# Performance work log

Hardware: AMD Instinct MI355X
Metric: run time of the kernel (lower is better)

## Reference

```python
import jax, jax.numpy as jnp
import numpy as np

EPS_NORM = 1e-12


def _sage_layer(h, src, dst, n_dst, W_self, W_neigh, b):
    # DGL SAGEConv(mean) on a bipartite block: dst nodes = first n_dst src nodes.
    h_dst = h[:n_dst]
    msgs = h[src]                                              # [E, d] irregular gather
    s = jax.ops.segment_sum(msgs, dst, num_segments=n_dst)    # [n_dst, d]
    cnt = jax.ops.segment_sum(jnp.ones((src.shape[0],), h.dtype), dst, num_segments=n_dst)
    agg = s / jnp.maximum(cnt, 1.0)[:, None]                   # mean over in-neighbors (0-deg -> 0)
    out = h_dst @ W_self + agg @ W_neigh + b
    out = jax.nn.relu(out)                                     # activation=F.relu
    nrm = jnp.maximum(jnp.linalg.norm(out, axis=1, keepdims=True), EPS_NORM)
    return out / nrm                                           # norm=F.normalize


def setup_inputs() -> dict:
    key = jax.random.key(0)
    ks = jax.random.split(key, 16)
    N0, N1, N2 = 200000, 50000, 10000
    E0, E1 = 800000, 160000
    F_IN, H, L = 128, 256, 32
    x = jax.random.uniform(ks[0], (N0, F_IN), dtype=jnp.float32)
    src0 = jax.random.randint(ks[1], (E0,), 0, N0, dtype=jnp.int32)
    dst0 = jax.random.randint(ks[2], (E0,), 0, N1, dtype=jnp.int32)
    src1 = jax.random.randint(ks[3], (E1,), 0, N1, dtype=jnp.int32)
    dst1 = jax.random.randint(ks[4], (E1,), 0, N2, dtype=jnp.int32)
    sc = 0.05
    return {
        "x": x,
        "W_self0": jax.random.normal(ks[5], (F_IN, H), jnp.float32) * sc,
        "W_neigh0": jax.random.normal(ks[6], (F_IN, H), jnp.float32) * sc,
        "b0": jnp.zeros((H,), jnp.float32),
        "W_self1": jax.random.normal(ks[7], (H, H), jnp.float32) * sc,
        "W_neigh1": jax.random.normal(ks[8], (H, H), jnp.float32) * sc,
        "b1": jnp.zeros((H,), jnp.float32),
        "W_mu": jax.random.normal(ks[9], (H, L), jnp.float32) * sc,
        "b_mu": jnp.zeros((L,), jnp.float32),
        "W_var": jax.random.normal(ks[10], (H, L), jnp.float32) * sc,
        "b_var": jnp.zeros((L,), jnp.float32),
        "src0": src0, "dst0": dst0, "src1": src1, "dst1": dst1,
        "n_dst0": N1, "n_dst1": N2,
    }


def reference(x, W_self0, W_neigh0, b0, W_self1, W_neigh1, b1,
              W_mu, b_mu, W_var, b_var,
              src0, dst0, src1, dst1, n_dst0, n_dst1):
    h = jnp.log(x + 1.0)
    h = _sage_layer(h, src0, dst0, n_dst0, W_self0, W_neigh0, b0)
    h = _sage_layer(h, src1, dst1, n_dst1, W_self1, W_neigh1, b1)
    z_loc = h @ W_mu + b_mu
    z_scale = jnp.exp(h @ W_var + b_var) + 1e-6
    return (z_loc, z_scale)
```

## Files before the change

kernel.cpp:

```cpp
#include <hip/hip_runtime.h>
#include <math.h>

#define DEVI static __device__ __forceinline__

typedef __attribute__((ext_vector_type(8))) short s16x8;
typedef __attribute__((ext_vector_type(4))) float f32x4;

constexpr int CH = 4096;
constexpr int PADS = 3840;

DEVI float bf2f(unsigned short u) {
  union { unsigned int i; float f; } v; v.i = ((unsigned int)u) << 16; return v.f;
}
DEVI unsigned short f2bf(float f) {
  union { float f; unsigned int i; } v; v.f = f;
  return (unsigned short)((v.i + 0x7fffu + ((v.i >> 16) & 1u)) >> 16);
}

DEVI float fast_log1p(float x) {
  float t = x + 1.0f;
  float l;
  asm("v_log_f32 %0, %1" : "=v"(l) : "v"(t));
  return l * 0.6931471805599453f;
}

DEVI void log1p_span(const float* __restrict__ x, unsigned short* __restrict__ h0,
                     int lo, int hi, int blk, int nblk) {
  int bs = blockDim.x;
  int stride = nblk * bs;
  for (int i = lo + blk * bs + threadIdx.x; i < hi; i += stride) {
    float4 v = ((const float4*)x)[i];
    ushort4 o;
    o.x = f2bf(fast_log1p(v.x)); o.y = f2bf(fast_log1p(v.y));
    o.z = f2bf(fast_log1p(v.z)); o.w = f2bf(fast_log1p(v.w));
    ((ushort4*)h0)[i] = o;
  }
}

__global__ __launch_bounds__(256) void front_k(const int* __restrict__ dst0, int E0,
                                               const int* __restrict__ dst1, int E1,
                                               unsigned* __restrict__ gh, int B0, int B1,
                                               const float* __restrict__ Ws0, const float* __restrict__ Wn0,
                                               const float* __restrict__ Ws1, const float* __restrict__ Wn1,
                                               const float* __restrict__ Wmu, const float* __restrict__ Wvar,
                                               unsigned short* __restrict__ T0s, unsigned short* __restrict__ T0n,
                                               unsigned short* __restrict__ T1s, unsigned short* __restrict__ T1n,
                                               unsigned short* __restrict__ Thead,
                                               unsigned short* __restrict__ h1z, int N0, int N1,
                                               const float* __restrict__ x, unsigned short* __restrict__ h0,
                                               int lo, int hi, int LA) {
  __shared__ unsigned h[256];
  int b = blockIdx.x;
  int t = threadIdx.x;
  int BH = B0 + B1;
  if (b < BH) {
    bool L1 = b >= B0;
    const int* dst = L1 ? dst1 : dst0;
    int E = L1 ? E1 : E0;
    int base = L1 ? b - B0 : b;
    unsigned* out = L1 ? gh + 256 * B0 : gh;
    int B = L1 ? B1 : B0;
    h[t] = 0;
    __syncthreads();
    int e0 = base * CH, eend = min(e0 + CH, E);
    for (int i = e0 + t; i < eend; i += 256) atomicAdd(&h[((unsigned)dst[i]) >> 8], 1u);
    __syncthreads();
    out[t * B + base] = h[t];
  } else if (b < BH + 256) {
    if (b == BH) {
      if (t < 64) ((unsigned*)h0)[(size_t)N0 * 64 + t] = 0u;
      if (t < 128) ((unsigned*)h1z)[(size_t)N1 * 128 + t] = 0u;
    }
    int i = (b - BH) * 256 + t;
    if (i < 32768) {
      int hh = i >> 7, k = i & 127;
      T0s[i] = f2bf(Ws0[k * 256 + hh]);
      T0n[i] = f2bf(Wn0[k * 256 + hh]);
    }
    if (i < 65536) {
      int hh = i >> 8, k = i & 255;
      T1s[i] = f2bf(Ws1[k * 256 + hh]);
      T1n[i] = f2bf(Wn1[k * 256 + hh]);
    }
    if (i < 16384) {
      int c = i >> 8, k = i & 255;
      Thead[i] = f2bf(c < 32 ? Wmu[k * 32 + c] : Wvar[k * 32 + (c - 32)]);
    }
  } else {
    log1p_span(x, h0, lo, hi, b - BH - 256, LA);
  }
}

__global__ __launch_bounds__(256) void scan_sums_k(const unsigned* __restrict__ a, int NB,
                                                   unsigned* __restrict__ part,
                                                   const float* __restrict__ x, unsigned short* __restrict__ h0,
                                                   int lo, int hi, int LB) {
  __shared__ unsigned sm[256];
  int b = blockIdx.x, t = threadIdx.x;
  if (b >= NB) { log1p_span(x, h0, lo, hi, b - NB, LB); return; }
  sm[t] = a[b * 256 + t];
  __syncthreads();
  for (int o = 128; o > 0; o >>= 1) {
    if (t < o) sm[t] += sm[t + o];
    __syncthreads();
  }
  if (t == 0) part[b] = sm[0];
}

__global__ __launch_bounds__(256) void scan_write_k(unsigned* __restrict__ a, int NB,
                                                    const unsigned* __restrict__ part,
                                                    const float* __restrict__ x, unsigned short* __restrict__ h0,
                                                    int lo, int hi, int LC) {
  __shared__ unsigned sm[256];
  int b = blockIdx.x, t = threadIdx.x;
  if (b >= NB) { log1p_span(x, h0, lo, hi, b - NB, LC); return; }
  unsigned pv = (t < NB) ? part[t] : 0u;
  sm[t] = pv;
  __syncthreads();
  for (int o = 1; o < 256; o <<= 1) {
    unsigned xv = (t >= o) ? sm[t - o] : 0u;
    __syncthreads();
    sm[t] += xv;
    __syncthreads();
  }
  unsigned pb = (b == 0) ? 0u : sm[b - 1];
  __syncthreads();
  unsigned v = a[b * 256 + t];
  sm[t] = v;
  __syncthreads();
  for (int o = 1; o < 256; o <<= 1) {
    unsigned xv = (t >= o) ? sm[t - o] : 0u;
    __syncthreads();
    sm[t] += xv;
    __syncthreads();
  }
  a[b * 256 + t] = pb + sm[t] - v;
}

__global__ __launch_bounds__(1024) void scatter2_k(const int* __restrict__ src0, const int* __restrict__ dst0, int E0,
                                                   const int* __restrict__ src1, const int* __restrict__ dst1, int E1,
                                                   const unsigned* __restrict__ gh, int B0, int B1,
                                                   uint2* __restrict__ tmp,
                                                   const float* __restrict__ x, unsigned short* __restrict__ h0,
                                                   int lo, int hi, int LS) {
  __shared__ unsigned cur[256];
  int b = blockIdx.x;
  int NB = B0 + B1;
  if (b >= NB) { log1p_span(x, h0, lo, hi, b - NB, LS); return; }
  bool L1 = b >= B0;
  const int* dst = L1 ? dst1 : dst0;
  const int* src = L1 ? src1 : src0;
  int E = L1 ? E1 : E0;
  int base = L1 ? b - B0 : b;
  const unsigned* g = L1 ? gh + 256 * B0 : gh;
  int B = L1 ? B1 : B0;
  int t = threadIdx.x;
  if (t < 256) cur[t] = g[t * B + base];
  __syncthreads();
  int e0 = base * CH, eend = min(e0 + CH, E);
  for (int i = e0 + t; i < eend; i += 1024) {
    int d = dst[i];
    unsigned p = atomicAdd(&cur[((unsigned)d) >> 8], 1u);
    tmp[p] = make_uint2((unsigned)d, (unsigned)src[i]);
  }
}

__global__ __launch_bounds__(1024) void finalize_k(const uint2* __restrict__ tmp, const unsigned* __restrict__ gh,
                                                   int B0, int B1, int N1, int N2,
                                                   unsigned* __restrict__ off, unsigned* __restrict__ cnt,
                                                   int* __restrict__ ss, int QB0, int QB1,
                                                   int sent0, int sent1,
                                                   const float* __restrict__ x, unsigned short* __restrict__ h0,
                                                   int lo, int hi, int LF) {
  __shared__ unsigned h[256];
  __shared__ unsigned sm[256];
  __shared__ unsigned co[256];
  int q = blockIdx.x;
  int QF = QB0 + QB1;
  if (q >= QF) { log1p_span(x, h0, lo, hi, q - QF, LF); return; }
  bool L1 = q >= QB0;
  int Nd = L1 ? N2 : N1;
  int qb = L1 ? q - QB0 : q;
  const unsigned* g = L1 ? gh + 256 * B0 : gh;
  int B = L1 ? B1 : B0;
  int t = threadIdx.x;
  unsigned bstart = g[qb * B];
  unsigned bend = g[(qb + 1) * B];
  unsigned nbk = bend - bstart;
  unsigned pbase = bstart + (unsigned)q * PADS;

  if (t < 256) h[t] = 0;
  __syncthreads();
  for (unsigned i = t; i < nbk; i += 1024) atomicAdd(&h[tmp[bstart + i].x & 255u], 1u);
  __syncthreads();
  unsigned v = 0, vpad = 0;
  if (t < 256) {
    v = h[t];
    vpad = (v + 15u) & ~15u;
    sm[t] = vpad;
  }
  __syncthreads();
  for (int o = 1; o < 256; o <<= 1) {
    unsigned xv = 0;
    if (t < 256 && t >= o) xv = sm[t - o];
    __syncthreads();
    if (t < 256) sm[t] += xv;
    __syncthreads();
  }
  if (t < 256) {
    unsigned myoff = pbase + sm[t] - vpad;
    int dl = qb * 256 + t;
    if (dl < Nd) {
      int dg = (L1 ? N1 : 0) + dl;
      off[dg] = myoff;
      cnt[dg] = v;
    }
    co[t] = myoff;
    int sent = L1 ? sent1 : sent0;
    for (unsigned j = v; j < vpad; ++j) ss[myoff + j] = sent;
  }
  __syncthreads();
  for (unsigned i = t; i < nbk; i += 1024) {
    uint2 e = tmp[bstart + i];
    unsigned p = atomicAdd(&co[e.x & 255u], 1u);
    ss[p] = (int)e.y;
  }
}

template <int UL, int PL>
DEVI void gstep(const unsigned short* __restrict__ hsrc, const int* __restrict__ ss,
                unsigned base, int half, int c32, float* fa) {
  constexpr int F = PL * 32;
  int sv[UL];
#pragma unroll
  for (int u = 0; u < UL; ++u) sv[u] = ss[base + 2 * u + half];
  if constexpr (PL == 4) {
    uint2 v[UL];
#pragma unroll
    for (int u = 0; u < UL; ++u) v[u] = *(const uint2*)&hsrc[(size_t)sv[u] * F + c32 * 4];
#pragma unroll
    for (int u = 0; u < UL; ++u) {
      fa[0] += bf2f((unsigned short)(v[u].x & 0xffffu));
      fa[1] += bf2f((unsigned short)(v[u].x >> 16));
      fa[2] += bf2f((unsigned short)(v[u].y & 0xffffu));
      fa[3] += bf2f((unsigned short)(v[u].y >> 16));
    }
  } else {
    uint4 v[UL];
#pragma unroll
    for (int u = 0; u < UL; ++u) v[u] = *(const uint4*)&hsrc[(size_t)sv[u] * F + c32 * 8];
#pragma unroll
    for (int u = 0; u < UL; ++u) {
      fa[0] += bf2f((unsigned short)(v[u].x & 0xffffu));
      fa[1] += bf2f((unsigned short)(v[u].x >> 16));
      fa[2] += bf2f((unsigned short)(v[u].y & 0xffffu));
      fa[3] += bf2f((unsigned short)(v[u].y >> 16));
      fa[4] += bf2f((unsigned short)(v[u].z & 0xffffu));
      fa[5] += bf2f((unsigned short)(v[u].z >> 16));
      fa[6] += bf2f((unsigned short)(v[u].w & 0xffffu));
      fa[7] += bf2f((unsigned short)(v[u].w >> 16));
    }
  }
}

template <int F>
__global__ __launch_bounds__(256) void aggregate_k(const unsigned short* __restrict__ hsrc,
                                                   const int* __restrict__ ss,
                                                   const unsigned* __restrict__ off,
                                                   const unsigned* __restrict__ cnt,
                                                   unsigned short* __restrict__ agg, int M) {
  constexpr int PL = F / 32;
  int w = threadIdx.x >> 6, l = threadIdx.x & 63;
  int half = l >> 5, c32 = l & 31;
  int d = blockIdx.x * 4 + w;
  if (d >= M) return;
  unsigned o = off[d];
  int n = (int)cnt[d];
  int npad = (n + 15) & ~15;
  float fa[PL];
#pragma unroll
  for (int f = 0; f < PL; ++f) fa[f] = 0.f;

  for (int i = 0; i < npad; i += 16) gstep<8, PL>(hsrc, ss, o + i, half, c32, fa);

#pragma unroll
  for (int f = 0; f < PL; ++f) fa[f] += __shfl_xor(fa[f], 32, 64);

  float inv = 1.0f / (float)((n > 0) ? n : 1);
  if (l < 32) {
    if constexpr (PL == 4) {
      uint2 ov;
      ov.x = (unsigned)f2bf(fa[0] * inv) | ((unsigned)f2bf(fa[1] * inv) << 16);
      ov.y = (unsigned)f2bf(fa[2] * inv) | ((unsigned)f2bf(fa[3] * inv) << 16);
      *(uint2*)&agg[(size_t)d * F + c32 * 4] = ov;
    } else {
      uint4 ov;
      ov.x = (unsigned)f2bf(fa[0] * inv) | ((unsigned)f2bf(fa[1] * inv) << 16);
      ov.y = (unsigned)f2bf(fa[2] * inv) | ((unsigned)f2bf(fa[3] * inv) << 16);
      ov.z = (unsigned)f2bf(fa[4] * inv) | ((unsigned)f2bf(fa[5] * inv) << 16);
      ov.w = (unsigned)f2bf(fa[6] * inv) | ((unsigned)f2bf(fa[7] * inv) << 16);
      *(uint4*)&agg[(size_t)d * F + c32 * 8] = ov;
    }
  }
}

template <int KD, bool HEAD>
__global__ __launch_bounds__(512) void layer_gemm_k(const unsigned short* __restrict__ Aself,
                                                    const unsigned short* __restrict__ Aagg,
                                                    const unsigned short* __restrict__ WtS,
                                                    const unsigned short* __restrict__ WtN,
                                                    const float* __restrict__ bias,
                                                    unsigned short* __restrict__ Hout,
                                                    const unsigned short* __restrict__ Thead,
                                                    const float* __restrict__ bmu, const float* __restrict__ bvar,
                                                    float* __restrict__ outp, int M) {
  __shared__ unsigned short At[128][40];
  __shared__ unsigned short Bt[256][40];
  __shared__ float rowsq[4][128];
  __shared__ float rowtot[128];
  __shared__ unsigned short h2t[HEAD ? 128 : 1][HEAD ? 264 : 1];

  int tid = threadIdx.x;
  int w = tid >> 6, l = tid & 63;
  int wr = w >> 2, wc = w & 3;
  int m0 = blockIdx.x * 128;

  f32x4 acc[4][4];
#pragma unroll
  for (int rt = 0; rt < 4; ++rt)
#pragma unroll
    for (int ct = 0; ct < 4; ++ct) acc[rt][ct] = (f32x4)(0.f);

  for (int s = 0; s < 2; ++s) {
    const unsigned short* A = s ? Aagg : Aself;
    const unsigned short* Wt = s ? WtN : WtS;
    for (int k0 = 0; k0 < KD; k0 += 32) {
      {
        int r = tid >> 2, c8 = (tid & 3) << 3;
        int gr = m0 + r;
        uint4 v = make_uint4(0, 0, 0, 0);
        if (gr < M) v = *(const uint4*)&A[(size_t)gr * KD + k0 + c8];
        *(uint4*)&At[r][c8] = v;
      }
#pragma unroll
      for (int rr = 0; rr < 2; ++rr) {
        int r = (tid >> 2) + (rr << 7), c8 = (tid & 3) << 3;
        uint4 v = *(const uint4*)&Wt[(size_t)r * KD + k0 + c8];
        *(uint4*)&Bt[r][c8] = v;
      }
      __syncthreads();
      s16x8 a[4], b[4];
#pragma unroll
      for (int rt = 0; rt < 4; ++rt) a[rt] = *(const s16x8*)&At[wr * 64 + rt * 16 + (l & 15)][(l >> 4) * 8];
#pragma unroll
      for (int ct = 0; ct < 4; ++ct) b[ct] = *(const s16x8*)&Bt[wc * 64 + ct * 16 + (l & 15)][(l >> 4) * 8];
#pragma unroll
      for (int rt = 0; rt < 4; ++rt)
#pragma unroll
        for (int ct = 0; ct < 4; ++ct)
          acc[rt][ct] = __builtin_amdgcn_mfma_f32_16x16x32_bf16(a[rt], b[ct], acc[rt][ct], 0, 0, 0);
      __syncthreads();
    }
  }

  float pr[4][4];
#pragma unroll
  for (int rt = 0; rt < 4; ++rt)
#pragma unroll
    for (int j = 0; j < 4; ++j) pr[rt][j] = 0.f;
#pragma unroll
  for (int rt = 0; rt < 4; ++rt)
#pragma unroll
    for (int ct = 0; ct < 4; ++ct) {
      int c = wc * 64 + ct * 16 + (l & 15);
      float bv = bias[c];
#pragma unroll
      for (int j = 0; j < 4; ++j) {
        float vv = acc[rt][ct][j] + bv;
        vv = fmaxf(vv, 0.f);
        acc[rt][ct][j] = vv;
        pr[rt][j] += vv * vv;
      }
    }
#pragma unroll
  for (int rt = 0; rt < 4; ++rt)
#pragma unroll
    for (int j = 0; j < 4; ++j) {
      float p = pr[rt][j];
      for (int m = 1; m < 16; m <<= 1) p += __shfl_xor(p, m, 64);
      pr[rt][j] = p;
    }
  if ((l & 15) == 0) {
#pragma unroll
    for (int rt = 0; rt < 4; ++rt)
#pragma unroll
      for (int j = 0; j < 4; ++j) rowsq[wc][wr * 64 + rt * 16 + (l >> 4) * 4 + j] = pr[rt][j];
  }
  __syncthreads();
  if (tid < 128) rowtot[tid] = rowsq[0][tid] + rowsq[1][tid] + rowsq[2][tid] + rowsq[3][tid];
  __syncthreads();

  if constexpr (!HEAD) {
#pragma unroll
    for (int rt = 0; rt < 4; ++rt) {
      int rbase = wr * 64 + rt * 16 + (l >> 4) * 4;
#pragma unroll
      for (int j = 0; j < 4; ++j) {
        int r = rbase + j;
        int gr = m0 + r;
        if (gr < M) {
          float inv = 1.0f / fmaxf(sqrtf(rowtot[r]), 1e-12f);
#pragma unroll
          for (int ct = 0; ct < 4; ++ct) {
            int c = wc * 64 + ct * 16 + (l & 15);
            Hout[(size_t)gr * 256 + c] = f2bf(acc[rt][ct][j] * inv);
          }
        }
      }
    }
  } else {
#pragma unroll
    for (int rt = 0; rt < 4; ++rt) {
      int rbase = wr * 64 + rt * 16 + (l >> 4) * 4;
#pragma unroll
      for (int j = 0; j < 4; ++j) {
        int r = rbase + j;
        float inv = 1.0f / fmaxf(sqrtf(rowtot[r]), 1e-12f);
#pragma unroll
        for (int ct = 0; ct < 4; ++ct) {
          int c = wc * 64 + ct * 16 + (l & 15);
          h2t[r][c] = f2bf(acc[rt][ct][j] * inv);
        }
      }
    }
    __syncthreads();

    const int arow = wr * 64 + (l & 15);
    const int kk = (l >> 4) * 8;
    f32x4 hacc[4];
#pragma unroll
    for (int rt = 0; rt < 4; ++rt) hacc[rt] = (f32x4)(0.f);
#pragma unroll
    for (int k0 = 0; k0 < 256; k0 += 32) {
      s16x8 ha[4];
#pragma unroll
      for (int rt = 0; rt < 4; ++rt) ha[rt] = *(const s16x8*)&h2t[arow + rt * 16][k0 + kk];
      s16x8 hb = *(const s16x8*)&Thead[(size_t)(wc * 16 + (l & 15)) * 256 + k0 + kk];
#pragma unroll
      for (int rt = 0; rt < 4; ++rt)
        hacc[rt] = __builtin_amdgcn_mfma_f32_16x16x32_bf16(ha[rt], hb, hacc[rt], 0, 0, 0);
    }
    const int c = wc * 16 + (l & 15);
    const float hbias = (c < 32) ? bmu[c] : bvar[c - 32];
#pragma unroll
    for (int rt = 0; rt < 4; ++rt)
#pragma unroll
      for (int j = 0; j < 4; ++j) {
        int gr = m0 + wr * 64 + rt * 16 + (l >> 4) * 4 + j;
        if (gr < M) {
          float val = hacc[rt][j] + hbias;
          if (c < 32)
            outp[(size_t)gr * 32 + c] = val;
          else
            outp[(size_t)M * 32 + (size_t)gr * 32 + (c - 32)] = expf(val) + 1e-6f;
        }
      }
  }
}

extern "C" void kernel_launch(void* const* d_in, const int* in_sizes, int n_in,
                              void* d_out, int out_size, void* d_ws, size_t ws_size,
                              hipStream_t stream) {
  const float* x    = (const float*)d_in[0];
  const float* Ws0  = (const float*)d_in[1];
  const float* Wn0  = (const float*)d_in[2];
  const float* b0   = (const float*)d_in[3];
  const float* Ws1  = (const float*)d_in[4];
  const float* Wn1  = (const float*)d_in[5];
  const float* b1   = (const float*)d_in[6];
  const float* Wmu  = (const float*)d_in[7];
  const float* bmu  = (const float*)d_in[8];
  const float* Wvar = (const float*)d_in[9];
  const float* bvar = (const float*)d_in[10];
  const int* src0   = (const int*)d_in[11];
  const int* dst0   = (const int*)d_in[12];
  const int* src1   = (const int*)d_in[13];
  const int* dst1   = (const int*)d_in[14];

  const int N0 = in_sizes[0] / 128;
  const int E0 = in_sizes[11];
  const int E1 = in_sizes[13];
  const int N1 = 50000, N2 = 10000;
  const int M = N1 + N2;

  char* ws = (char*)d_ws;
  size_t o = 0;
  auto take = [&](size_t b) -> char* {
    size_t cur = (o + 255) & ~(size_t)255;
    o = cur + b;
    return ws + cur;
  };
  unsigned short* h0    = (unsigned short*)take((size_t)(N0 + 1) * 128 * 2);
  unsigned short* agg0  = (unsigned short*)take((size_t)N1 * 128 * 2);
  unsigned short* h1    = (unsigned short*)take((size_t)(N1 + 1) * 256 * 2);
  unsigned short* agg1  = (unsigned short*)take((size_t)N2 * 256 * 2);
  unsigned short* T0s   = (unsigned short*)take(256 * 128 * 2);
  unsigned short* T0n   = (unsigned short*)take(256 * 128 * 2);
  unsigned short* T1s   = (unsigned short*)take(256 * 256 * 2);
  unsigned short* T1n   = (unsigned short*)take(256 * 256 * 2);
  unsigned short* Thead = (unsigned short*)take(64 * 256 * 2);

  int B0 = (E0 + CH - 1) / CH;
  int B1 = (E1 + CH - 1) / CH;
  int NB = B0 + B1;
  int G  = 256 * NB;
  int QB0 = (N1 + 255) / 256;
  int QB1 = (N2 + 255) / 256;
  int QF  = QB0 + QB1;

  unsigned* gh   = (unsigned*)take((size_t)G * 4);
  unsigned* off  = (unsigned*)take((size_t)M * 4);
  unsigned* cnt  = (unsigned*)take((size_t)M * 4);
  unsigned* part = (unsigned*)take(256 * 4);
  uint2* tmp = (uint2*)take((size_t)(E0 + E1) * 8);
  int* ss = (int*)take(((size_t)(E0 + E1) + (size_t)QF * PADS) * 4);
  (void)ws_size;

  const int n4 = N0 * 128 / 4;
  const int c1 = n4 * 8 / 100, c2 = n4 * 16 / 100, c3 = n4 * 25 / 100, c4 = n4 * 60 / 100;
  const int LA = 768, LBs = 768, LC = 768;
  const int LS = 384, LF = 384;

  front_k<<<NB + 256 + LA, 256, 0, stream>>>(dst0, E0, dst1, E1, gh, B0, B1,
                                             Ws0, Wn0, Ws1, Wn1, Wmu, Wvar,
                                             T0s, T0n, T1s, T1n, Thead,
                                             h1, N0, N1,
                                             x, h0, 0, c1, LA);

  scan_sums_k<<<NB + LBs, 256, 0, stream>>>(gh, NB, part, x, h0, c1, c2, LBs);
  scan_write_k<<<NB + LC, 256, 0, stream>>>(gh, NB, part, x, h0, c2, c3, LC);

  scatter2_k<<<NB + LS, 1024, 0, stream>>>(src0, dst0, E0, src1, dst1, E1, gh, B0, B1, tmp,
                                           x, h0, c3, c4, LS);
  finalize_k<<<QF + LF, 1024, 0, stream>>>(tmp, gh, B0, B1, N1, N2, off, cnt, ss, QB0, QB1,
                                           N0, N1,
                                           x, h0, c4, n4, LF);

  aggregate_k<128><<<(N1 + 3) / 4, 256, 0, stream>>>(h0, ss, off, cnt, agg0, N1);
  layer_gemm_k<128, false><<<(N1 + 127) / 128, 512, 0, stream>>>(h0, agg0, T0s, T0n, b0,
                                                                 h1, nullptr, nullptr, nullptr, nullptr, N1);

  aggregate_k<256><<<(N2 + 3) / 4, 256, 0, stream>>>(h1, ss, off + N1, cnt + N1, agg1, N2);
  layer_gemm_k<256, true><<<(N2 + 127) / 128, 512, 0, stream>>>(h1, agg1, T1s, T1n, b1,
                                                                nullptr, Thead, bmu, bvar, (float*)d_out, N2);
}
```

Measured before the change: 149.7 us.

## Split layer-0 aggregation and GEMM into staggered fused kernels for overlap

The layer-0 finalize, aggregation and GEMM are split into row ranges and packed into heterogeneous kernels. Finalize of the first destination blocks runs alone. The second launch finishes the remaining finalize work while aggregating those first rows. The GEMM for those rows then runs alongside aggregation of the remaining rows, and the GEMM for the remaining tiles follows. The log1p work is pulled out of finalize and redistributed across the earlier front kernels. The aim is to fill idle CUs during small serial stages and drop a launch, but it adds more launches for layer 0 and relies on a fixed split constant (QH=118).

```diff
diff --git a/kernel.cpp b/kernel.cpp
--- a/kernel.cpp
+++ b/kernel.cpp
@@ -34,6 +34,78 @@
     o.x = f2bf(fast_log1p(v.x)); o.y = f2bf(fast_log1p(v.y));
     o.z = f2bf(fast_log1p(v.z)); o.w = f2bf(fast_log1p(v.w));
     ((ushort4*)h0)[i] = o;
+  }
+}
+
+template <int UL, int PL>
+DEVI void gstep(const unsigned short* __restrict__ hsrc, const int* __restrict__ ss,
+                unsigned base, int half, int c32, float* fa) {
+  constexpr int F = PL * 32;
+  int sv[UL];
+#pragma unroll
+  for (int u = 0; u < UL; ++u) sv[u] = ss[base + 2 * u + half];
+  if constexpr (PL == 4) {
+    uint2 v[UL];
+#pragma unroll
+    for (int u = 0; u < UL; ++u) v[u] = *(const uint2*)&hsrc[(size_t)sv[u] * F + c32 * 4];
+#pragma unroll
+    for (int u = 0; u < UL; ++u) {
+      fa[0] += bf2f((unsigned short)(v[u].x & 0xffffu));
+      fa[1] += bf2f((unsigned short)(v[u].x >> 16));
+      fa[2] += bf2f((unsigned short)(v[u].y & 0xffffu));
+      fa[3] += bf2f((unsigned short)(v[u].y >> 16));
+    }
+  } else {
+    uint4 v[UL];
+#pragma unroll
+    for (int u = 0; u < UL; ++u) v[u] = *(const uint4*)&hsrc[(size_t)sv[u] * F + c32 * 8];
+#pragma unroll
+    for (int u = 0; u < UL; ++u) {
+      fa[0] += bf2f((unsigned short)(v[u].x & 0xffffu));
+      fa[1] += bf2f((unsigned short)(v[u].x >> 16));
+      fa[2] += bf2f((unsigned short)(v[u].y & 0xffffu));
+      fa[3] += bf2f((unsigned short)(v[u].y >> 16));
+      fa[4] += bf2f((unsigned short)(v[u].z & 0xffffu));
+      fa[5] += bf2f((unsigned short)(v[u].z >> 16));
+      fa[6] += bf2f((unsigned short)(v[u].w & 0xffffu));
+      fa[7] += bf2f((unsigned short)(v[u].w >> 16));
+    }
+  }
+}
+
+template <int F>
+DEVI void agg_wave(const unsigned short* __restrict__ hsrc, const int* __restrict__ ss,
+                   const unsigned* __restrict__ off, const unsigned* __restrict__ cnt,
+                   unsigned short* __restrict__ agg, int d, int l) {
+  constexpr int PL = F / 32;
+  int half = l >> 5, c32 = l & 31;
+  unsigned o = off[d];
+  int n = (int)cnt[d];
+  int npad = (n + 15) & ~15;
+  float fa[PL];
+#pragma unroll
+  for (int f = 0; f < PL; ++f) fa[f] = 0.f;
+
+  for (int i = 0; i < npad; i += 16) gstep<8, PL>(hsrc, ss, o + i, half, c32, fa);
+
+#pragma unroll
+  for (int f = 0; f < PL; ++f) fa[f] += __shfl_xor(fa[f], 32, 64);
+
+  float inv = 1.0f / (float)((n > 0) ? n : 1);
+  if (l < 32) {
+    if constexpr (PL == 4) {
+      uint2 ov;
+      ov.x = (unsigned)f2bf(fa[0] * inv) | ((unsigned)f2bf(fa[1] * inv) << 16);
+      ov.y = (unsigned)f2bf(fa[2] * inv) | ((unsigned)f2bf(fa[3] * inv) << 16);
+      *(uint2*)&agg[(size_t)d * F + c32 * 4] = ov;
+    } else {
+      uint4 ov;
+      ov.x = (unsigned)f2bf(fa[0] * inv) | ((unsigned)f2bf(fa[1] * inv) << 16);
+      ov.y = (unsigned)f2bf(fa[2] * inv) | ((unsigned)f2bf(fa[3] * inv) << 16);
+      ov.z = (unsigned)f2bf(fa[4] * inv) | ((unsigned)f2bf(fa[5] * inv) << 16);
+      ov.w = (unsigned)f2bf(fa[6] * inv) | ((unsigned)f2bf(fa[7] * inv) << 16);
+      *(uint4*)&agg[(size_t)d * F + c32 * 8] = ov;
+    }
   }
 }
 
@@ -165,25 +237,29 @@
   }
 }
 
-__global__ __launch_bounds__(1024) void finalize_k(const uint2* __restrict__ tmp, const unsigned* __restrict__ gh,
-                                                   int B0, int B1, int N1, int N2,
-                                                   unsigned* __restrict__ off, unsigned* __restrict__ cnt,
-                                                   int* __restrict__ ss, int QB0, int QB1,
-                                                   int sent0, int sent1,
-                                                   const float* __restrict__ x, unsigned short* __restrict__ h0,
-                                                   int lo, int hi, int LF) {
+__global__ __launch_bounds__(1024) void finagg_k(const uint2* __restrict__ tmp, const unsigned* __restrict__ gh,
+                                                 int B0, int B1, int N1, int N2,
+                                                 unsigned* __restrict__ off, unsigned* __restrict__ cnt,
+                                                 int* __restrict__ ss, int QB0, int QB1,
+                                                 int sent0, int sent1, int qlo, int nfin,
+                                                 const unsigned short* __restrict__ h0agg,
+                                                 unsigned short* __restrict__ agg0, int aggd0, int aggM) {
   __shared__ unsigned h[256];
   __shared__ unsigned sm[256];
   __shared__ unsigned co[256];
-  int q = blockIdx.x;
-  int QF = QB0 + QB1;
-  if (q >= QF) { log1p_span(x, h0, lo, hi, q - QF, LF); return; }
+  int b = blockIdx.x;
+  int t = threadIdx.x;
+  if (b >= nfin) {
+    int d = aggd0 + (b - nfin) * 16 + (t >> 6);
+    if (d < aggM) agg_wave<128>(h0agg, ss, off, cnt, agg0, d, t & 63);
+    return;
+  }
+  int q = qlo + b;
   bool L1 = q >= QB0;
   int Nd = L1 ? N2 : N1;
   int qb = L1 ? q - QB0 : q;
   const unsigned* g = L1 ? gh + 256 * B0 : gh;
   int B = L1 ? B1 : B0;
-  int t = threadIdx.x;
   unsigned bstart = g[qb * B];
   unsigned bend = g[(qb + 1) * B];
   unsigned nbk = bend - bstart;
@@ -227,81 +303,15 @@
   }
 }
 
-template <int UL, int PL>
-DEVI void gstep(const unsigned short* __restrict__ hsrc, const int* __restrict__ ss,
-                unsigned base, int half, int c32, float* fa) {
-  constexpr int F = PL * 32;
-  int sv[UL];
-#pragma unroll
-  for (int u = 0; u < UL; ++u) sv[u] = ss[base + 2 * u + half];
-  if constexpr (PL == 4) {
-    uint2 v[UL];
-#pragma unroll
-    for (int u = 0; u < UL; ++u) v[u] = *(const uint2*)&hsrc[(size_t)sv[u] * F + c32 * 4];
-#pragma unroll
-    for (int u = 0; u < UL; ++u) {
-      fa[0] += bf2f((unsigned short)(v[u].x & 0xffffu));
-      fa[1] += bf2f((unsigned short)(v[u].x >> 16));
-      fa[2] += bf2f((unsigned short)(v[u].y & 0xffffu));
-      fa[3] += bf2f((unsigned short)(v[u].y >> 16));
-    }
-  } else {
-    uint4 v[UL];
-#pragma unroll
-    for (int u = 0; u < UL; ++u) v[u] = *(const uint4*)&hsrc[(size_t)sv[u] * F + c32 * 8];
-#pragma unroll
-    for (int u = 0; u < UL; ++u) {
-      fa[0] += bf2f((unsigned short)(v[u].x & 0xffffu));
-      fa[1] += bf2f((unsigned short)(v[u].x >> 16));
-      fa[2] += bf2f((unsigned short)(v[u].y & 0xffffu));
-      fa[3] += bf2f((unsigned short)(v[u].y >> 16));
-      fa[4] += bf2f((unsigned short)(v[u].z & 0xffffu));
-      fa[5] += bf2f((unsigned short)(v[u].z >> 16));
-      fa[6] += bf2f((unsigned short)(v[u].w & 0xffffu));
-      fa[7] += bf2f((unsigned short)(v[u].w >> 16));
-    }
-  }
-}
-
 template <int F>
 __global__ __launch_bounds__(256) void aggregate_k(const unsigned short* __restrict__ hsrc,
                                                    const int* __restrict__ ss,
                                                    const unsigned* __restrict__ off,
                                                    const unsigned* __restrict__ cnt,
                                                    unsigned short* __restrict__ agg, int M) {
-  constexpr int PL = F / 32;
-  int w = threadIdx.x >> 6, l = threadIdx.x & 63;
-  int half = l >> 5, c32 = l & 31;
-  int d = blockIdx.x * 4 + w;
+  int d = blockIdx.x * 4 + (threadIdx.x >> 6);
   if (d >= M) return;
-  unsigned o = off[d];
-  int n = (int)cnt[d];
-  int npad = (n + 15) & ~15;
-  float fa[PL];
-#pragma unroll
-  for (int f = 0; f < PL; ++f) fa[f] = 0.f;
-
-  for (int i = 0; i < npad; i += 16) gstep<8, PL>(hsrc, ss, o + i, half, c32, fa);
-
-#pragma unroll
-  for (int f = 0; f < PL; ++f) fa[f] += __shfl_xor(fa[f], 32, 64);
-
-  float inv = 1.0f / (float)((n > 0) ? n : 1);
-  if (l < 32) {
-    if constexpr (PL == 4) {
-      uint2 ov;
-      ov.x = (unsigned)f2bf(fa[0] * inv) | ((unsigned)f2bf(fa[1] * inv) << 16);
-      ov.y = (unsigned)f2bf(fa[2] * inv) | ((unsigned)f2bf(fa[3] * inv) << 16);
-      *(uint2*)&agg[(size_t)d * F + c32 * 4] = ov;
-    } else {
-      uint4 ov;
-      ov.x = (unsigned)f2bf(fa[0] * inv) | ((unsigned)f2bf(fa[1] * inv) << 16);
-      ov.y = (unsigned)f2bf(fa[2] * inv) | ((unsigned)f2bf(fa[3] * inv) << 16);
-      ov.z = (unsigned)f2bf(fa[4] * inv) | ((unsigned)f2bf(fa[5] * inv) << 16);
-      ov.w = (unsigned)f2bf(fa[6] * inv) | ((unsigned)f2bf(fa[7] * inv) << 16);
-      *(uint4*)&agg[(size_t)d * F + c32 * 8] = ov;
-    }
-  }
+  agg_wave<F>(hsrc, ss, off, cnt, agg, d, threadIdx.x & 63);
 }
 
 template <int KD, bool HEAD>
@@ -313,7 +323,11 @@
                                                     unsigned short* __restrict__ Hout,
                                                     const unsigned short* __restrict__ Thead,
                                                     const float* __restrict__ bmu, const float* __restrict__ bvar,
-                                                    float* __restrict__ outp, int M) {
+                                                    float* __restrict__ outp, int M,
+                                                    int tile0, int ngemm,
+                                                    const int* __restrict__ ss,
+                                                    const unsigned* __restrict__ off,
+                                                    const unsigned* __restrict__ cnt, int aggd0) {
   __shared__ unsigned short At[128][40];
   __shared__ unsigned short Bt[256][40];
   __shared__ float rowsq[4][128];
@@ -321,9 +335,14 @@
   __shared__ unsigned short h2t[HEAD ? 128 : 1][HEAD ? 264 : 1];
 
   int tid = threadIdx.x;
+  if (blockIdx.x >= ngemm) {
+    int d = aggd0 + (blockIdx.x - ngemm) * 8 + (tid >> 6);
+    if (d < M) agg_wave<KD>(Aself, ss, off, cnt, (unsigned short*)Aagg, d, tid & 63);
+    return;
+  }
   int w = tid >> 6, l = tid & 63;
   int wr = w >> 2, wc = w & 3;
-  int m0 = blockIdx.x * 128;
+  int m0 = (tile0 + blockIdx.x) * 128;
 
   f32x4 acc[4][4];
 #pragma unroll
@@ -527,9 +546,13 @@
   (void)ws_size;
 
   const int n4 = N0 * 128 / 4;
-  const int c1 = n4 * 8 / 100, c2 = n4 * 16 / 100, c3 = n4 * 25 / 100, c4 = n4 * 60 / 100;
-  const int LA = 768, LBs = 768, LC = 768;
-  const int LS = 384, LF = 384;
+  const int c1 = n4 * 20 / 100, c2 = n4 * 35 / 100, c3 = n4 * 50 / 100;
+  const int LA = 768, LBs = 768, LC = 768, LS = 384;
+
+  const int QH = 118;
+  const int RH = QH * 256;
+  const int TH = RH / 128;
+  const int T0cnt = (N1 + 127) / 128;
 
   front_k<<<NB + 256 + LA, 256, 0, stream>>>(dst0, E0, dst1, E1, gh, B0, B1,
                                              Ws0, Wn0, Ws1, Wn1, Wmu, Wvar,
@@ -541,16 +564,23 @@
   scan_write_k<<<NB + LC, 256, 0, stream>>>(gh, NB, part, x, h0, c2, c3, LC);
 
   scatter2_k<<<NB + LS, 1024, 0, stream>>>(src0, dst0, E0, src1, dst1, E1, gh, B0, B1, tmp,
-                                           x, h0, c3, c4, LS);
-  finalize_k<<<QF + LF, 1024, 0, stream>>>(tmp, gh, B0, B1, N1, N2, off, cnt, ss, QB0, QB1,
-                                           N0, N1,
-                                           x, h0, c4, n4, LF);
-
-  aggregate_k<128><<<(N1 + 3) / 4, 256, 0, stream>>>(h0, ss, off, cnt, agg0, N1);
-  layer_gemm_k<128, false><<<(N1 + 127) / 128, 512, 0, stream>>>(h0, agg0, T0s, T0n, b0,
-                                                                 h1, nullptr, nullptr, nullptr, nullptr, N1);
+                                           x, h0, c3, n4, LS);
+
+  finagg_k<<<QH, 1024, 0, stream>>>(tmp, gh, B0, B1, N1, N2, off, cnt, ss, QB0, QB1,
+                                    N0, N1, 0, QH, h0, agg0, 0, 0);
+  int aggAblk = RH / 16;
+  finagg_k<<<(QF - QH) + aggAblk, 1024, 0, stream>>>(tmp, gh, B0, B1, N1, N2, off, cnt, ss, QB0, QB1,
+                                                     N0, N1, QH, QF - QH, h0, agg0, 0, RH);
+  int aggBblk = (N1 - RH + 7) / 8;
+  layer_gemm_k<128, false><<<TH + aggBblk, 512, 0, stream>>>(h0, agg0, T0s, T0n, b0,
+                                                             h1, nullptr, nullptr, nullptr, nullptr, N1,
+                                                             0, TH, ss, off, cnt, RH);
+  layer_gemm_k<128, false><<<T0cnt - TH, 512, 0, stream>>>(h0, agg0, T0s, T0n, b0,
+                                                           h1, nullptr, nullptr, nullptr, nullptr, N1,
+                                                           TH, T0cnt - TH, nullptr, nullptr, nullptr, 0);
 
   aggregate_k<256><<<(N2 + 3) / 4, 256, 0, stream>>>(h1, ss, off + N1, cnt + N1, agg1, N2);
   layer_gemm_k<256, true><<<(N2 + 127) / 128, 512, 0, stream>>>(h1, agg1, T1s, T1n, b1,
-                                                                nullptr, Thead, bmu, bvar, (float*)d_out, N2);
-}
+                                                                nullptr, Thead, bmu, bvar, (float*)d_out, N2,
+                                                                0, (N2 + 127) / 128, nullptr, nullptr, nullptr, 0);
+}
```

Measured after the change: 169.8 us. 1.13x slower.
